# Kernel optimization log

Hardware: AMD Instinct MI355X
Metric: run time of the kernel (lower is better)

## Reference

```python
import jax, jax.numpy as jnp
import numpy as np

B, N = 2, 8192

PARAM_SHAPES = {
    'down0_w': (32, 3), 'down0_b': (32,),
    'sc1_w1': (32, 35), 'sc1_b1': (32,), 'sc1_w2': (64, 32), 'sc1_b2': (64,),
    'sc2_w1': (64, 67), 'sc2_b1': (64,), 'sc2_w2': (128, 64), 'sc2_b2': (128,),
    'sc3_w1': (128, 131), 'sc3_b1': (128,), 'sc3_w2': (192, 128), 'sc3_b2': (192,),
    'sc4_w1': (192, 195), 'sc4_b1': (192,), 'sc4_w2': (192, 192), 'sc4_b2': (192,),
    'up4_w1': (192, 195), 'up4_b1': (192,), 'up4_w2': (192, 384), 'up4_b2': (192,),
    'up3_w1': (128, 195), 'up3_b1': (128,), 'up3_w2': (128, 256), 'up3_b2': (128,),
    'up2_w1': (64, 131), 'up2_b1': (64,), 'up2_w2': (64, 128), 'up2_b2': (64,),
    'up1_w1': (32, 67), 'up1_b1': (32,), 'up1_w2': (32, 64), 'up1_b2': (32,),
}
PNAMES = list(PARAM_SHAPES.keys())


def _fps(xyz, m):
    # xyz [N,3] -> [m] int32 farthest-point-sample indices (deterministic, start at point 0)
    def body(dmin, _):
        nxt = jnp.argmax(dmin)
        d = jnp.sum((xyz - xyz[nxt]) ** 2, -1)
        return jnp.minimum(dmin, d), nxt.astype(jnp.int32)
    d0 = jnp.sum((xyz - xyz[0]) ** 2, -1)
    _, rest = jax.lax.scan(body, d0, None, length=m - 1)
    return jnp.concatenate([jnp.zeros((1,), jnp.int32), rest])


def _gather(pts, idx):
    # pts [B,N,C], idx [B,...] -> [B,...,C]
    return jax.vmap(lambda p, i: p[i])(pts, idx)


def _ball_query(new_xyz, xyz, radius, k):
    # first-k points within radius, invalid slots filled with the first valid index
    d2 = jnp.sum((new_xyz[:, :, None, :] - xyz[:, None, :, :]) ** 2, -1)  # [B,M,N]
    n = xyz.shape[1]
    order = jnp.where(d2 <= radius * radius, jnp.arange(n)[None, None, :], n)
    idx = jnp.argsort(order, axis=-1)[..., :k]
    valid = jnp.take_along_axis(order, idx, -1) < n
    return jnp.where(valid, idx, idx[..., :1])


def _knn(query, ref, k):
    d2 = jnp.sum((query[:, :, None, :] - ref[:, None, :, :]) ** 2, -1)  # [B,Nq,Nr]
    _, idx = jax.lax.top_k(-d2, k)
    return idx


def _mlp(h, w, b):
    # pointwise shared MLP layer with ReLU on channel-last tensor
    return jax.nn.relu(jnp.einsum('...c,oc->...o', h, w) + b)


def _set_conv(xyz, feat, npoint, radius, k, w1, b1, w2, b2):
    # PointNet++-style SetConv: FPS -> ball-query group -> shared MLP -> max-pool
    fps_idx = jax.vmap(_fps, (0, None))(xyz, npoint)          # [B,M]
    new_xyz = _gather(xyz, fps_idx)                            # [B,M,3]
    gi = _ball_query(new_xyz, xyz, radius, k)                  # [B,M,k]
    h = jnp.concatenate([_gather(xyz, gi) - new_xyz[:, :, None, :], _gather(feat, gi)], -1)
    h = _mlp(_mlp(h, w1, b1), w2, b2)                          # [B,M,k,Cout]
    return new_xyz, fps_idx, jnp.max(h, axis=2)


def _set_upconv(s_xyz, d_xyz, s_feat, d_feat, k, w1, b1, w2, b2):
    # FlowNet3D-style SetUpConv: kNN from dense to sparse -> MLP -> max-pool -> fuse with dense feat
    gi = _knn(d_xyz, s_xyz, k)                                 # [B,Nd,k]
    h = jnp.concatenate([_gather(s_xyz, gi) - d_xyz[:, :, None, :], _gather(s_feat, gi)], -1)
    pooled = jnp.max(_mlp(h, w1, b1), axis=2)                  # [B,Nd,m1]
    return _mlp(jnp.concatenate([pooled, d_feat], -1), w2, b2)


def _encoder(pc, feat, p):
    xyz = jnp.transpose(pc, (0, 2, 1))                         # [B,N,3]
    f0 = _mlp(jnp.transpose(feat, (0, 2, 1)), p['down0_w'], p['down0_b'])  # [B,N,32]
    xyz1, i1, f1 = _set_conv(xyz, f0, 2048, 0.5, 16, p['sc1_w1'], p['sc1_b1'], p['sc1_w2'], p['sc1_b2'])
    xyz2, i2, f2 = _set_conv(xyz1, f1, 512, 1.0, 16, p['sc2_w1'], p['sc2_b1'], p['sc2_w2'], p['sc2_b2'])
    xyz3, i3, f3 = _set_conv(xyz2, f2, 128, 2.0, 16, p['sc3_w1'], p['sc3_b1'], p['sc3_w2'], p['sc3_b2'])
    xyz4, i4, f4 = _set_conv(xyz3, f3, 64, 4.0, 16, p['sc4_w1'], p['sc4_b1'], p['sc4_w2'], p['sc4_b2'])
    u3 = _set_upconv(xyz4, xyz3, f4, f3, 8, p['up4_w1'], p['up4_b1'], p['up4_w2'], p['up4_b2'])
    u2 = _set_upconv(xyz3, xyz2, u3, f2, 8, p['up3_w1'], p['up3_b1'], p['up3_w2'], p['up3_b2'])
    u1 = _set_upconv(xyz2, xyz1, u2, f1, 8, p['up2_w1'], p['up2_b1'], p['up2_w2'], p['up2_b2'])
    u0 = _set_upconv(xyz1, xyz, u1, f0, 8, p['up1_w1'], p['up1_b1'], p['up1_w2'], p['up1_b2'])
    return (xyz1, xyz2, xyz3), (i1, i2, i3), (u0, u1, u2, u3)


def setup_inputs() -> dict:
    key = jax.random.key(0)
    ks = jax.random.split(key, 2 + len(PNAMES))
    inp = {
        'pc': jax.random.normal(ks[0], (B, 3, N), jnp.float32),
        'feat': jax.random.normal(ks[1], (B, 3, N), jnp.float32),
    }
    for i, name in enumerate(PNAMES):
        inp[name] = jax.random.normal(ks[2 + i], PARAM_SHAPES[name], jnp.float32) * 0.05
    return inp


def reference(pc, feat, down0_w, down0_b, sc1_w1, sc1_b1, sc1_w2, sc1_b2, sc2_w1, sc2_b1, sc2_w2, sc2_b2, sc3_w1, sc3_b1, sc3_w2, sc3_b2, sc4_w1, sc4_b1, sc4_w2, sc4_b2, up4_w1, up4_b1, up4_w2, up4_b2, up3_w1, up3_b1, up3_w2, up3_b2, up2_w1, up2_b1, up2_w2, up2_b2, up1_w1, up1_b1, up1_w2, up1_b2):
    # GenFlow_unit.forward with gts[0] is None -> pure encoder path
    loc = locals()
    p = {k: loc[k] for k in PNAMES}
    (x1, x2, x3), (i1, i2, i3), (u0, u1, u2, u3) = _encoder(pc, feat, p)
    t = lambda a: jnp.transpose(a, (0, 2, 1))  # back to torch channel-first convention
    return (t(x1), t(x2), t(x3), i1, i2, i3, t(u0), t(u1), t(u2), t(u3))
```

## Files before the change

kernel.cpp:

```cpp
#include <hip/hip_runtime.h>
#include <hip/hip_bf16.h>
#include <cstdint>

#define DEV __device__ __forceinline__

typedef float f32x2 __attribute__((ext_vector_type(2)));

DEV float sqdist(float ax, float ay, float az, float bx, float by, float bz) {
    float dx = __fsub_rn(ax, bx), dy = __fsub_rn(ay, by), dz = __fsub_rn(az, bz);
    return __fadd_rn(__fadd_rn(__fmul_rn(dx, dx), __fmul_rn(dy, dy)), __fmul_rn(dz, dz));
}

DEV f32x2 sqdist2(f32x2 ax, f32x2 ay, f32x2 az, float bx, float by, float bz) {
#pragma clang fp contract(off)
    f32x2 dx = ax - bx, dy = ay - by, dz = az - bz;
    return (dx * dx + dy * dy) + dz * dz;
}

DEV unsigned short f2bf(float f) {
    unsigned int u = __float_as_uint(f);
    u += 0x7fffu + ((u >> 16) & 1u);
    return (unsigned short)(u >> 16);
}

DEV float bf2f(unsigned short u) { return __uint_as_float(((unsigned int)u) << 16); }

template <int CTRL>
DEV int dpp_i(int v) { return __builtin_amdgcn_update_dpp(v, v, CTRL, 0xf, 0xf, false); }
template <int CTRL>
DEV float dpp_f(float v) { return __int_as_float(dpp_i<CTRL>(__float_as_int(v))); }

enum : int {
    O_X1 = 0, O_X2 = 12288, O_X3 = 15360,
    O_I1 = 16128, O_I2 = 20224, O_I3 = 21248,
    O_U0 = 21504, O_U1 = 545792, O_U2 = 807936, O_U3 = 939008
};

__global__ __launch_bounds__(256) void k_init(const float* __restrict__ pc,
                                              const float* __restrict__ feat,
                                              const float* __restrict__ w0,
                                              const float* __restrict__ b0,
                                              float* __restrict__ xyz,
                                              unsigned short* __restrict__ f0) {
    const int N = 8192;
    int i = blockIdx.x * blockDim.x + threadIdx.x;
    if (i >= 2 * N) return;
    int b = i / N, n = i % N;
    float fx0 = feat[(b * 3 + 0) * N + n];
    float fx1 = feat[(b * 3 + 1) * N + n];
    float fx2 = feat[(b * 3 + 2) * N + n];
    xyz[i * 3 + 0] = pc[(b * 3 + 0) * N + n];
    xyz[i * 3 + 1] = pc[(b * 3 + 1) * N + n];
    xyz[i * 3 + 2] = pc[(b * 3 + 2) * N + n];
#pragma unroll
    for (int o = 0; o < 32; o++) {
        float acc = b0[o];
        acc = fmaf(w0[o * 3 + 0], fx0, acc);
        acc = fmaf(w0[o * 3 + 1], fx1, acc);
        acc = fmaf(w0[o * 3 + 2], fx2, acc);
        f0[(size_t)i * 32 + o] = f2bf(fmaxf(acc, 0.f));
    }
}

template <int N, int M, int T>
__global__ __launch_bounds__(T, 1) void k_fps(const float* __restrict__ xyz,
                                              int* __restrict__ idx_out) {
    constexpr int P = N / T;
    constexpr int P2 = P / 2;
    constexpr int W = T / 64;
    int b = blockIdx.x;
    const float* X = xyz + (size_t)b * N * 3;
    int t = threadIdx.x;
    __shared__ float sx[N], sy[N], sz[N];
    __shared__ unsigned long long skey[3];
    f32x2 px[P2], py[P2], pz[P2], dmin[P2];
    float c0x = X[0], c0y = X[1], c0z = X[2];
#pragma unroll
    for (int i = 0; i < P2; i++) {
        int p0 = (2 * i) * T + t, p1 = (2 * i + 1) * T + t;
        px[i] = f32x2{X[p0 * 3 + 0], X[p1 * 3 + 0]};
        py[i] = f32x2{X[p0 * 3 + 1], X[p1 * 3 + 1]};
        pz[i] = f32x2{X[p0 * 3 + 2], X[p1 * 3 + 2]};
        sx[p0] = px[i].x; sy[p0] = py[i].x; sz[p0] = pz[i].x;
        sx[p1] = px[i].y; sy[p1] = py[i].y; sz[p1] = pz[i].y;
        dmin[i] = sqdist2(px[i], py[i], pz[i], c0x, c0y, c0z);
    }
    if (t == 0) {
        idx_out[b * M] = 0;
        skey[0] = 0; skey[1] = 0; skey[2] = 0;
    }
    __syncthreads();
    int jm = 1;
    for (int j = 1; j < M; j++) {
        f32x2 m2[P2];
#pragma unroll
        for (int i = 0; i < P2; i++) m2[i] = dmin[i];
#pragma unroll
        for (int s = P2 / 2; s >= 1; s >>= 1)
#pragma unroll
            for (int i = 0; i < s; i++) m2[i] = __builtin_elementwise_max(m2[i], m2[i + s]);
        float bv = fmaxf(m2[0].x, m2[0].y);
        int ii[P];
#pragma unroll
        for (int i = 0; i < P; i++)
            ii[i] = (dmin[i >> 1][i & 1] == bv) ? (i * T + t) : 0x7fffffff;
#pragma unroll
        for (int s = P / 2; s >= 1; s >>= 1)
#pragma unroll
            for (int i = 0; i < s; i++) ii[i] = min(ii[i], ii[i + s]);
        int bi = ii[0];
        float bw = bv;
        bw = fmaxf(bw, dpp_f<0x121>(bw));
        bw = fmaxf(bw, dpp_f<0x122>(bw));
        bw = fmaxf(bw, dpp_f<0x124>(bw));
        bw = fmaxf(bw, dpp_f<0x128>(bw));
        bw = fmaxf(bw, dpp_f<0x142>(bw));
        bw = fmaxf(bw, dpp_f<0x143>(bw));
        float bvw = __int_as_float(__builtin_amdgcn_readlane(__float_as_int(bw), 63));
        unsigned int im = (bv == bvw) ? (unsigned int)bi : 0xffffffffu;
        im = min(im, (unsigned int)dpp_i<0x121>((int)im));
        im = min(im, (unsigned int)dpp_i<0x122>((int)im));
        im = min(im, (unsigned int)dpp_i<0x124>((int)im));
        im = min(im, (unsigned int)dpp_i<0x128>((int)im));
        im = min(im, (unsigned int)dpp_i<0x142>((int)im));
        im = min(im, (unsigned int)dpp_i<0x143>((int)im));
        int biw = __builtin_amdgcn_readlane((int)im, 63);
        int gi;
        if constexpr (W > 1) {
            unsigned long long key =
                ((unsigned long long)__float_as_uint(bvw) << 32) | (unsigned int)~biw;
            if ((t & 63) == 0) atomicMax(&skey[jm], key);
            __syncthreads();
            unsigned long long gk = skey[jm];
            gi = (int)~(unsigned int)gk;
            if (t == 0) skey[jm == 0 ? 2 : jm - 1] = 0;
            jm = (jm == 2) ? 0 : jm + 1;
        } else {
            gi = biw;
        }
        if (t == 0) idx_out[b * M + j] = gi;
        float cx = sx[gi], cy = sy[gi], cz = sz[gi];
#pragma unroll
        for (int i = 0; i < P2; i++)
            dmin[i] = __builtin_elementwise_min(
                dmin[i], sqdist2(px[i], py[i], pz[i], cx, cy, cz));
    }
}

__global__ __launch_bounds__(256) void k_gather(const float* __restrict__ xyz_src,
                                                const int* __restrict__ idx,
                                                float* __restrict__ xyz_dst,
                                                int NS, int M) {
    int i = blockIdx.x * blockDim.x + threadIdx.x;
    if (i >= 2 * M) return;
    int b = i / M;
    int id = idx[i] & (NS - 1);
    xyz_dst[i * 3 + 0] = xyz_src[((size_t)b * NS + id) * 3 + 0];
    xyz_dst[i * 3 + 1] = xyz_src[((size_t)b * NS + id) * 3 + 1];
    xyz_dst[i * 3 + 2] = xyz_src[((size_t)b * NS + id) * 3 + 2];
}

template <int NS, int CF, int CMID, int COUT>
__global__ __launch_bounds__(128) void k_setconv(
    const float* __restrict__ X, const unsigned short* __restrict__ F,
    const float* __restrict__ C, const float* __restrict__ w1,
    const float* __restrict__ b1, const float* __restrict__ w2,
    const float* __restrict__ b2, unsigned short* __restrict__ fout,
    float r2, int M) {
    constexpr int CIN = 3 + CF;
    constexpr int K = 16;
    constexpr int M8 = CMID / 8;
    constexpr int O8 = COUT / 8;
    int q = blockIdx.x, b = blockIdx.y;
    int blk = b * M + q;
    const float* Xb = X + (size_t)b * NS * 3;
    const unsigned short* Fb = F + (size_t)b * NS * CF;
    int tid = threadIdx.x;
    __shared__ int s_n[K];
    __shared__ int s_cnt;
    __shared__ float s_h[K][CIN];
    __shared__ float s_mid[K][CMID];
    __shared__ float s_pool[2][COUT];
    float cx = C[(size_t)blk * 3 + 0], cy = C[(size_t)blk * 3 + 1], cz = C[(size_t)blk * 3 + 2];
    if (tid < 64) {
        int lane = tid;
        int cnt = 0;
        for (int base = 0; base < NS; base += 64) {
            int p = base + lane;
            float d2 = sqdist(Xb[p * 3], Xb[p * 3 + 1], Xb[p * 3 + 2], cx, cy, cz);
            bool in = (d2 <= r2);
            unsigned long long msk = __ballot(in);
            if (in) {
                int pos = cnt + __popcll(msk & ((1ull << lane) - 1ull));
                if (pos < K) s_n[pos] = p;
            }
            cnt += __popcll(msk);
            if (cnt >= K) break;
        }
        if (lane == 0) s_cnt = cnt < K ? cnt : K;
    }
    __syncthreads();
    int cnt = s_cnt;
    if (tid >= cnt && tid < K) s_n[tid] = s_n[0];
    __syncthreads();
    for (int tIdx = tid; tIdx < K * CIN; tIdx += 128) {
        int n = tIdx / CIN, c = tIdx % CIN;
        int gi = s_n[n];
        float v;
        if (c < 3) v = __fsub_rn(Xb[gi * 3 + c], (c == 0 ? cx : (c == 1 ? cy : cz)));
        else v = bf2f(Fb[(size_t)gi * CF + (c - 3)]);
        s_h[n][c] = v;
    }
    __syncthreads();
    int n = tid >> 3, sub = tid & 7;
#pragma unroll
    for (int j = 0; j < M8; j++) {
        int m = sub * M8 + j;
        float acc = b1[m];
#pragma unroll 4
        for (int c = 0; c < CIN; c++) acc = fmaf(w1[m * CIN + c], s_h[n][c], acc);
        s_mid[n][m] = fmaxf(acc, 0.f);
    }
    __syncthreads();
    float vals[O8];
#pragma unroll
    for (int j = 0; j < O8; j++) {
        int o = sub * O8 + j;
        float acc = b2[o];
#pragma unroll 4
        for (int c = 0; c < CMID; c++) acc = fmaf(w2[o * CMID + c], s_mid[n][c], acc);
        vals[j] = fmaxf(acc, 0.f);
    }
#pragma unroll
    for (int j = 0; j < O8; j++) {
        vals[j] = fmaxf(vals[j], __shfl_xor(vals[j], 8, 64));
        vals[j] = fmaxf(vals[j], __shfl_xor(vals[j], 16, 64));
        vals[j] = fmaxf(vals[j], __shfl_xor(vals[j], 32, 64));
    }
    int lw = tid & 63, wv = tid >> 6;
    if (lw < 8) {
#pragma unroll
        for (int j = 0; j < O8; j++) s_pool[wv][lw * O8 + j] = vals[j];
    }
    __syncthreads();
    if (tid < 8) {
#pragma unroll
        for (int j = 0; j < O8; j++) {
            int o = tid * O8 + j;
            fout[(size_t)blk * COUT + o] = f2bf(fmaxf(s_pool[0][o], s_pool[1][o]));
        }
    }
}

template <int S, int CS, int CMID, int CD, int COUT, bool TRANS>
__global__ __launch_bounds__(64) void k_upconv(
    const float* __restrict__ SX, const float* __restrict__ DX,
    const void* __restrict__ SFv, const unsigned short* __restrict__ DF,
    const float* __restrict__ w1, const float* __restrict__ b1,
    const float* __restrict__ w2, const float* __restrict__ b2,
    float* __restrict__ out, int o_off, int ND) {
    constexpr int K = 8;
    constexpr int CIN = 3 + CS;
    constexpr int CIN2 = CMID + CD;
    constexpr int M8 = CMID / 8;
    int q = blockIdx.x, b = blockIdx.y;
    int blk = b * ND + q;
    int lane = threadIdx.x;
    const float* SXb = SX + (size_t)b * S * 3;
    float qx = DX[(size_t)blk * 3], qy = DX[(size_t)blk * 3 + 1], qz = DX[(size_t)blk * 3 + 2];
    __shared__ int s_k[K];
    __shared__ float s_h[K][CIN];
    __shared__ float s_in2[CIN2];
    float bd[K];
    int bi[K];
#pragma unroll
    for (int i = 0; i < K; i++) { bd[i] = 3.0e38f; bi[i] = 0x7fffffff; }
    for (int p = lane; p < S; p += 64) {
        float d2 = sqdist(SXb[p * 3], SXb[p * 3 + 1], SXb[p * 3 + 2], qx, qy, qz);
        if (d2 < bd[K - 1] || (d2 == bd[K - 1] && p < bi[K - 1])) {
            bd[K - 1] = d2; bi[K - 1] = p;
#pragma unroll
            for (int j = K - 1; j > 0; j--) {
                bool sw = (bd[j] < bd[j - 1]) || (bd[j] == bd[j - 1] && bi[j] < bi[j - 1]);
                if (sw) {
                    float tv = bd[j]; bd[j] = bd[j - 1]; bd[j - 1] = tv;
                    int ti = bi[j]; bi[j] = bi[j - 1]; bi[j - 1] = ti;
                }
            }
        }
    }
    for (int r = 0; r < K; r++) {
        float vv = bd[0]; int vi = bi[0];
#pragma unroll
        for (int m = 1; m < 64; m <<= 1) {
            float ov = __shfl_xor(vv, m, 64);
            int oi = __shfl_xor(vi, m, 64);
            if (ov < vv || (ov == vv && oi < vi)) { vv = ov; vi = oi; }
        }
        if (lane == 0) s_k[r] = vi;
        if (vi == bi[0]) {
#pragma unroll
            for (int j = 0; j < K - 1; j++) { bd[j] = bd[j + 1]; bi[j] = bi[j + 1]; }
            bd[K - 1] = 3.0e38f; bi[K - 1] = 0x7fffffff;
        }
    }
    __syncthreads();
    for (int tIdx = lane; tIdx < K * CIN; tIdx += 64) {
        int n = tIdx / CIN, c = tIdx % CIN;
        int gi = s_k[n];
        float v;
        if (c < 3) v = __fsub_rn(SXb[gi * 3 + c], (c == 0 ? qx : (c == 1 ? qy : qz)));
        else if (TRANS) v = ((const float*)SFv)[((size_t)b * CS + (c - 3)) * S + gi];
        else v = bf2f(((const unsigned short*)SFv)[((size_t)b * S + gi) * CS + (c - 3)]);
        s_h[n][c] = v;
    }
    for (int c = lane; c < CD; c += 64) s_in2[CMID + c] = bf2f(DF[(size_t)blk * CD + c]);
    __syncthreads();
    int n = lane >> 3, sub = lane & 7;
    float vals[M8];
#pragma unroll
    for (int j = 0; j < M8; j++) {
        int m = sub * M8 + j;
        float acc = b1[m];
#pragma unroll 4
        for (int c = 0; c < CIN; c++) acc = fmaf(w1[m * CIN + c], s_h[n][c], acc);
        vals[j] = fmaxf(acc, 0.f);
    }
#pragma unroll
    for (int j = 0; j < M8; j++) {
        vals[j] = fmaxf(vals[j], __shfl_xor(vals[j], 8, 64));
        vals[j] = fmaxf(vals[j], __shfl_xor(vals[j], 16, 64));
        vals[j] = fmaxf(vals[j], __shfl_xor(vals[j], 32, 64));
    }
    if (lane < 8) {
#pragma unroll
        for (int j = 0; j < M8; j++) s_in2[lane * M8 + j] = vals[j];
    }
    __syncthreads();
    for (int o = lane; o < COUT; o += 64) {
        float acc = b2[o];
#pragma unroll 4
        for (int c = 0; c < CIN2; c++) acc = fmaf(w2[o * CIN2 + c], s_in2[c], acc);
        out[o_off + ((size_t)b * COUT + o) * ND + q] = fmaxf(acc, 0.f);
    }
}

__global__ __launch_bounds__(256) void k_finalize(
    const float* __restrict__ xyz1, const float* __restrict__ xyz2,
    const float* __restrict__ xyz3, const int* __restrict__ idx1,
    const int* __restrict__ idx2, const int* __restrict__ idx3,
    float* __restrict__ out) {
    int i = blockIdx.x * blockDim.x + threadIdx.x;
    const float* xs;
    const int* is;
    int M, ox, oi, j;
    if (i < 4096) { xs = xyz1; is = idx1; M = 2048; ox = O_X1; oi = O_I1; j = i; }
    else if (i < 5120) { xs = xyz2; is = idx2; M = 512; ox = O_X2; oi = O_I2; j = i - 4096; }
    else if (i < 5376) { xs = xyz3; is = idx3; M = 128; ox = O_X3; oi = O_I3; j = i - 5120; }
    else return;
    int b = j / M, m = j % M;
    out[ox + (b * 3 + 0) * M + m] = xs[j * 3 + 0];
    out[ox + (b * 3 + 1) * M + m] = xs[j * 3 + 1];
    out[ox + (b * 3 + 2) * M + m] = xs[j * 3 + 2];
    out[oi + j] = (float)is[j];
}

extern "C" void kernel_launch(void* const* d_in, const int* in_sizes, int n_in,
                              void* d_out, int out_size, void* d_ws, size_t ws_size,
                              hipStream_t stream) {
    const float* pc = (const float*)d_in[0];
    const float* feat = (const float*)d_in[1];
    const float* w0 = (const float*)d_in[2];
    const float* b0v = (const float*)d_in[3];
    const float* sc1w1 = (const float*)d_in[4];  const float* sc1b1 = (const float*)d_in[5];
    const float* sc1w2 = (const float*)d_in[6];  const float* sc1b2 = (const float*)d_in[7];
    const float* sc2w1 = (const float*)d_in[8];  const float* sc2b1 = (const float*)d_in[9];
    const float* sc2w2 = (const float*)d_in[10]; const float* sc2b2 = (const float*)d_in[11];
    const float* sc3w1 = (const float*)d_in[12]; const float* sc3b1 = (const float*)d_in[13];
    const float* sc3w2 = (const float*)d_in[14]; const float* sc3b2 = (const float*)d_in[15];
    const float* sc4w1 = (const float*)d_in[16]; const float* sc4b1 = (const float*)d_in[17];
    const float* sc4w2 = (const float*)d_in[18]; const float* sc4b2 = (const float*)d_in[19];
    const float* up4w1 = (const float*)d_in[20]; const float* up4b1 = (const float*)d_in[21];
    const float* up4w2 = (const float*)d_in[22]; const float* up4b2 = (const float*)d_in[23];
    const float* up3w1 = (const float*)d_in[24]; const float* up3b1 = (const float*)d_in[25];
    const float* up3w2 = (const float*)d_in[26]; const float* up3b2 = (const float*)d_in[27];
    const float* up2w1 = (const float*)d_in[28]; const float* up2b1 = (const float*)d_in[29];
    const float* up2w2 = (const float*)d_in[30]; const float* up2b2 = (const float*)d_in[31];
    const float* up1w1 = (const float*)d_in[32]; const float* up1b1 = (const float*)d_in[33];
    const float* up1w2 = (const float*)d_in[34]; const float* up1b2 = (const float*)d_in[35];
    float* out = (float*)d_out;

    char* ws = (char*)d_ws;
    size_t off = 0;
    auto A = [&](size_t bytes) -> char* {
        char* p = ws + off;
        off += (bytes + 255) & ~(size_t)255;
        return p;
    };
    float* xyz  = (float*)A((size_t)2 * 8192 * 3 * 4);
    int* idx1   = (int*)A((size_t)2 * 2048 * 4);
    int* idx2   = (int*)A((size_t)2 * 512 * 4);
    int* idx3   = (int*)A((size_t)2 * 128 * 4);
    int* idx4   = (int*)A((size_t)2 * 64 * 4);
    float* xyz1 = (float*)A((size_t)2 * 2048 * 3 * 4);
    float* xyz2 = (float*)A((size_t)2 * 512 * 3 * 4);
    float* xyz3 = (float*)A((size_t)2 * 128 * 3 * 4);
    float* xyz4 = (float*)A((size_t)2 * 64 * 3 * 4);
    unsigned short* f0 = (unsigned short*)A((size_t)2 * 8192 * 32 * 2);
    unsigned short* f1 = (unsigned short*)A((size_t)2 * 2048 * 64 * 2);
    unsigned short* f2 = (unsigned short*)A((size_t)2 * 512 * 128 * 2);
    unsigned short* f3 = (unsigned short*)A((size_t)2 * 128 * 192 * 2);
    unsigned short* f4 = (unsigned short*)A((size_t)2 * 64 * 192 * 2);

    k_init<<<(2 * 8192 + 255) / 256, 256, 0, stream>>>(pc, feat, w0, b0v, xyz, f0);

    k_fps<8192, 2048, 512><<<2, 512, 0, stream>>>(xyz, idx1);
    k_gather<<<16, 256, 0, stream>>>(xyz, idx1, xyz1, 8192, 2048);
    k_setconv<8192, 32, 32, 64><<<dim3(2048, 2), 128, 0, stream>>>(
        xyz, f0, xyz1, sc1w1, sc1b1, sc1w2, sc1b2, f1, 0.25f, 2048);

    k_fps<2048, 512, 512><<<2, 512, 0, stream>>>(xyz1, idx2);
    k_gather<<<4, 256, 0, stream>>>(xyz1, idx2, xyz2, 2048, 512);
    k_setconv<2048, 64, 64, 128><<<dim3(512, 2), 128, 0, stream>>>(
        xyz1, f1, xyz2, sc2w1, sc2b1, sc2w2, sc2b2, f2, 1.0f, 512);

    k_fps<512, 128, 256><<<2, 256, 0, stream>>>(xyz2, idx3);
    k_gather<<<1, 256, 0, stream>>>(xyz2, idx3, xyz3, 512, 128);
    k_setconv<512, 128, 128, 192><<<dim3(128, 2), 128, 0, stream>>>(
        xyz2, f2, xyz3, sc3w1, sc3b1, sc3w2, sc3b2, f3, 4.0f, 128);

    k_fps<128, 64, 64><<<2, 64, 0, stream>>>(xyz3, idx4);
    k_gather<<<1, 128, 0, stream>>>(xyz3, idx4, xyz4, 128, 64);
    k_setconv<128, 192, 192, 192><<<dim3(64, 2), 128, 0, stream>>>(
        xyz3, f3, xyz4, sc4w1, sc4b1, sc4w2, sc4b2, f4, 16.0f, 64);

    k_upconv<64, 192, 192, 192, 192, false><<<dim3(128, 2), 64, 0, stream>>>(
        xyz4, xyz3, f4, f3, up4w1, up4b1, up4w2, up4b2, out, O_U3, 128);
    k_upconv<128, 192, 128, 128, 128, true><<<dim3(512, 2), 64, 0, stream>>>(
        xyz3, xyz2, out + O_U3, f2, up3w1, up3b1, up3w2, up3b2, out, O_U2, 512);
    k_upconv<512, 128, 64, 64, 64, true><<<dim3(2048, 2), 64, 0, stream>>>(
        xyz2, xyz1, out + O_U2, f1, up2w1, up2b1, up2w2, up2b2, out, O_U1, 2048);
    k_upconv<2048, 64, 32, 32, 32, true><<<dim3(8192, 2), 64, 0, stream>>>(
        xyz1, xyz, out + O_U1, f0, up1w1, up1b1, up1w2, up1b2, out, O_U0, 8192);

    k_finalize<<<(5376 + 255) / 256, 256, 0, stream>>>(
        xyz1, xyz2, xyz3, idx1, idx2, idx3, out);
}
```

Baseline: 4.047 ms.

## Fuse next-level FPS with current set-conv in one launch and use DPP kNN reductions

Merges the next level's farthest-point sampling and the current level's set-conv into one kernel. Two blocks run FPS while the remaining blocks each handle a set-conv centroid, so the serial FPS overlaps the set-conv work and launches are reduced. The level-3 FPS and gather are also moved ahead of the sc3 set-conv. Separately, the kNN top-k wave reduction in upconv now uses DPP min plus readlane instead of xor shuffles. The risks are that set-conv blocks now launch at 512 or 256 threads with only 128 active in the MLP, and that sizing shared memory to the larger FPS need limits occupancy.

Result: faster. 3.846 ms (-5.0%).

```diff
diff --git a/kernel.cpp b/kernel.cpp
--- a/kernel.cpp
+++ b/kernel.cpp
@@ -63,16 +63,16 @@
 }
 
 template <int N, int M, int T>
-__global__ __launch_bounds__(T, 1) void k_fps(const float* __restrict__ xyz,
-                                              int* __restrict__ idx_out) {
+DEV void fps_body(int b, int t, const float* __restrict__ xyz,
+                  int* __restrict__ idx_out, char* smem) {
     constexpr int P = N / T;
     constexpr int P2 = P / 2;
     constexpr int W = T / 64;
-    int b = blockIdx.x;
     const float* X = xyz + (size_t)b * N * 3;
-    int t = threadIdx.x;
-    __shared__ float sx[N], sy[N], sz[N];
-    __shared__ unsigned long long skey[3];
+    float* sx = (float*)smem;
+    float* sy = sx + N;
+    float* sz = sy + N;
+    unsigned long long* skey = (unsigned long long*)(smem + 12 * N);
     f32x2 px[P2], py[P2], pz[P2], dmin[P2];
     float c0x = X[0], c0y = X[1], c0z = X[2];
 #pragma unroll
@@ -147,6 +147,13 @@
     }
 }
 
+template <int N, int M, int T>
+__global__ __launch_bounds__(T, 1) void k_fps(const float* __restrict__ xyz,
+                                              int* __restrict__ idx_out) {
+    __shared__ __align__(16) char smem[12 * N + 24];
+    fps_body<N, M, T>(blockIdx.x, threadIdx.x, xyz, idx_out, smem);
+}
+
 __global__ __launch_bounds__(256) void k_gather(const float* __restrict__ xyz_src,
                                                 const int* __restrict__ idx,
                                                 float* __restrict__ xyz_dst,
@@ -161,26 +168,24 @@
 }
 
 template <int NS, int CF, int CMID, int COUT>
-__global__ __launch_bounds__(128) void k_setconv(
-    const float* __restrict__ X, const unsigned short* __restrict__ F,
-    const float* __restrict__ C, const float* __restrict__ w1,
-    const float* __restrict__ b1, const float* __restrict__ w2,
-    const float* __restrict__ b2, unsigned short* __restrict__ fout,
-    float r2, int M) {
+DEV void setconv_body(int q, int bb, int tid, int bdim,
+                      const float* __restrict__ X, const unsigned short* __restrict__ F,
+                      const float* __restrict__ C, const float* __restrict__ w1,
+                      const float* __restrict__ b1, const float* __restrict__ w2,
+                      const float* __restrict__ b2, unsigned short* __restrict__ fout,
+                      float r2, int M, char* smem) {
     constexpr int CIN = 3 + CF;
     constexpr int K = 16;
     constexpr int M8 = CMID / 8;
     constexpr int O8 = COUT / 8;
-    int q = blockIdx.x, b = blockIdx.y;
-    int blk = b * M + q;
-    const float* Xb = X + (size_t)b * NS * 3;
-    const unsigned short* Fb = F + (size_t)b * NS * CF;
-    int tid = threadIdx.x;
-    __shared__ int s_n[K];
-    __shared__ int s_cnt;
-    __shared__ float s_h[K][CIN];
-    __shared__ float s_mid[K][CMID];
-    __shared__ float s_pool[2][COUT];
+    int blk = bb * M + q;
+    const float* Xb = X + (size_t)bb * NS * 3;
+    const unsigned short* Fb = F + (size_t)bb * NS * CF;
+    int* s_n = (int*)smem;
+    int* s_cntp = (int*)(smem + 64);
+    float* s_h = (float*)(smem + 80);
+    float* s_mid = s_h + K * CIN;
+    float* s_pool = s_mid + K * CMID;
     float cx = C[(size_t)blk * 3 + 0], cy = C[(size_t)blk * 3 + 1], cz = C[(size_t)blk * 3 + 2];
     if (tid < 64) {
         int lane = tid;
@@ -197,58 +202,101 @@
             cnt += __popcll(msk);
             if (cnt >= K) break;
         }
-        if (lane == 0) s_cnt = cnt < K ? cnt : K;
-    }
-    __syncthreads();
-    int cnt = s_cnt;
+        if (lane == 0) *s_cntp = cnt < K ? cnt : K;
+    }
+    __syncthreads();
+    int cnt = *s_cntp;
     if (tid >= cnt && tid < K) s_n[tid] = s_n[0];
     __syncthreads();
-    for (int tIdx = tid; tIdx < K * CIN; tIdx += 128) {
+    for (int tIdx = tid; tIdx < K * CIN; tIdx += bdim) {
         int n = tIdx / CIN, c = tIdx % CIN;
         int gi = s_n[n];
         float v;
         if (c < 3) v = __fsub_rn(Xb[gi * 3 + c], (c == 0 ? cx : (c == 1 ? cy : cz)));
         else v = bf2f(Fb[(size_t)gi * CF + (c - 3)]);
-        s_h[n][c] = v;
-    }
-    __syncthreads();
-    int n = tid >> 3, sub = tid & 7;
-#pragma unroll
-    for (int j = 0; j < M8; j++) {
-        int m = sub * M8 + j;
-        float acc = b1[m];
+        s_h[n * CIN + c] = v;
+    }
+    __syncthreads();
+    if (tid < 128) {
+        int n = tid >> 3, sub = tid & 7;
+#pragma unroll
+        for (int j = 0; j < M8; j++) {
+            int m = sub * M8 + j;
+            float acc = b1[m];
 #pragma unroll 4
-        for (int c = 0; c < CIN; c++) acc = fmaf(w1[m * CIN + c], s_h[n][c], acc);
-        s_mid[n][m] = fmaxf(acc, 0.f);
-    }
-    __syncthreads();
-    float vals[O8];
-#pragma unroll
-    for (int j = 0; j < O8; j++) {
-        int o = sub * O8 + j;
-        float acc = b2[o];
+            for (int c = 0; c < CIN; c++) acc = fmaf(w1[m * CIN + c], s_h[n * CIN + c], acc);
+            s_mid[n * CMID + m] = fmaxf(acc, 0.f);
+        }
+    }
+    __syncthreads();
+    if (tid < 128) {
+        int n = tid >> 3, sub = tid & 7;
+        float vals[O8];
+#pragma unroll
+        for (int j = 0; j < O8; j++) {
+            int o = sub * O8 + j;
+            float acc = b2[o];
 #pragma unroll 4
-        for (int c = 0; c < CMID; c++) acc = fmaf(w2[o * CMID + c], s_mid[n][c], acc);
-        vals[j] = fmaxf(acc, 0.f);
-    }
-#pragma unroll
-    for (int j = 0; j < O8; j++) {
-        vals[j] = fmaxf(vals[j], __shfl_xor(vals[j], 8, 64));
-        vals[j] = fmaxf(vals[j], __shfl_xor(vals[j], 16, 64));
-        vals[j] = fmaxf(vals[j], __shfl_xor(vals[j], 32, 64));
-    }
-    int lw = tid & 63, wv = tid >> 6;
-    if (lw < 8) {
-#pragma unroll
-        for (int j = 0; j < O8; j++) s_pool[wv][lw * O8 + j] = vals[j];
+            for (int c = 0; c < CMID; c++) acc = fmaf(w2[o * CMID + c], s_mid[n * CMID + c], acc);
+            vals[j] = fmaxf(acc, 0.f);
+        }
+#pragma unroll
+        for (int j = 0; j < O8; j++) {
+            vals[j] = fmaxf(vals[j], __shfl_xor(vals[j], 8, 64));
+            vals[j] = fmaxf(vals[j], __shfl_xor(vals[j], 16, 64));
+            vals[j] = fmaxf(vals[j], __shfl_xor(vals[j], 32, 64));
+        }
+        int lw = tid & 63, wv = tid >> 6;
+        if (lw < 8) {
+#pragma unroll
+            for (int j = 0; j < O8; j++) s_pool[wv * COUT + lw * O8 + j] = vals[j];
+        }
     }
     __syncthreads();
     if (tid < 8) {
 #pragma unroll
         for (int j = 0; j < O8; j++) {
             int o = tid * O8 + j;
-            fout[(size_t)blk * COUT + o] = f2bf(fmaxf(s_pool[0][o], s_pool[1][o]));
-        }
+            fout[(size_t)blk * COUT + o] = f2bf(fmaxf(s_pool[o], s_pool[COUT + o]));
+        }
+    }
+}
+
+template <int NS, int CF, int CMID, int COUT>
+__global__ __launch_bounds__(128) void k_setconv(
+    const float* __restrict__ X, const unsigned short* __restrict__ F,
+    const float* __restrict__ C, const float* __restrict__ w1,
+    const float* __restrict__ b1, const float* __restrict__ w2,
+    const float* __restrict__ b2, unsigned short* __restrict__ fout,
+    float r2, int M) {
+    constexpr int K = 16;
+    constexpr int CIN = 3 + CF;
+    __shared__ __align__(16) char smem[80 + 4 * (K * CIN + K * CMID + 2 * COUT)];
+    setconv_body<NS, CF, CMID, COUT>(blockIdx.x, blockIdx.y, threadIdx.x, blockDim.x,
+                                     X, F, C, w1, b1, w2, b2, fout, r2, M, smem);
+}
+
+template <int N, int M, int T, int NS, int CF, int CMID, int COUT>
+__global__ __launch_bounds__(T, 1) void k_fps_sc(
+    const float* __restrict__ fxyz, int* __restrict__ idx_out,
+    const float* __restrict__ X, const unsigned short* __restrict__ F,
+    const float* __restrict__ C, const float* __restrict__ w1,
+    const float* __restrict__ b1, const float* __restrict__ w2,
+    const float* __restrict__ b2, unsigned short* __restrict__ fout,
+    float r2, int Msc) {
+    constexpr int K = 16;
+    constexpr int CIN = 3 + CF;
+    constexpr int FPS_B = 12 * N + 24;
+    constexpr int SC_B = 80 + 4 * (K * CIN + K * CMID + 2 * COUT);
+    constexpr int SB = FPS_B > SC_B ? FPS_B : SC_B;
+    __shared__ __align__(16) char smem[SB];
+    if (blockIdx.x < 2) {
+        fps_body<N, M, T>(blockIdx.x, threadIdx.x, fxyz, idx_out, smem);
+    } else {
+        int lin = blockIdx.x - 2;
+        int q = lin % Msc, bb = lin / Msc;
+        setconv_body<NS, CF, CMID, COUT>(q, bb, threadIdx.x, blockDim.x,
+                                         X, F, C, w1, b1, w2, b2, fout, r2, Msc, smem);
     }
 }
 
@@ -290,15 +338,25 @@
         }
     }
     for (int r = 0; r < K; r++) {
-        float vv = bd[0]; int vi = bi[0];
-#pragma unroll
-        for (int m = 1; m < 64; m <<= 1) {
-            float ov = __shfl_xor(vv, m, 64);
-            int oi = __shfl_xor(vi, m, 64);
-            if (ov < vv || (ov == vv && oi < vi)) { vv = ov; vi = oi; }
-        }
-        if (lane == 0) s_k[r] = vi;
-        if (vi == bi[0]) {
+        float vv = bd[0];
+        float bw = vv;
+        bw = fminf(bw, dpp_f<0x121>(bw));
+        bw = fminf(bw, dpp_f<0x122>(bw));
+        bw = fminf(bw, dpp_f<0x124>(bw));
+        bw = fminf(bw, dpp_f<0x128>(bw));
+        bw = fminf(bw, dpp_f<0x142>(bw));
+        bw = fminf(bw, dpp_f<0x143>(bw));
+        float vw = __int_as_float(__builtin_amdgcn_readlane(__float_as_int(bw), 63));
+        unsigned int im = (vv == vw) ? (unsigned int)bi[0] : 0xffffffffu;
+        im = min(im, (unsigned int)dpp_i<0x121>((int)im));
+        im = min(im, (unsigned int)dpp_i<0x122>((int)im));
+        im = min(im, (unsigned int)dpp_i<0x124>((int)im));
+        im = min(im, (unsigned int)dpp_i<0x128>((int)im));
+        im = min(im, (unsigned int)dpp_i<0x142>((int)im));
+        im = min(im, (unsigned int)dpp_i<0x143>((int)im));
+        int iw = __builtin_amdgcn_readlane((int)im, 63);
+        if (lane == 0) s_k[r] = iw;
+        if (iw == bi[0]) {
 #pragma unroll
             for (int j = 0; j < K - 1; j++) { bd[j] = bd[j + 1]; bi[j] = bi[j + 1]; }
             bd[K - 1] = 3.0e38f; bi[K - 1] = 0x7fffffff;
@@ -416,21 +474,16 @@
 
     k_fps<8192, 2048, 512><<<2, 512, 0, stream>>>(xyz, idx1);
     k_gather<<<16, 256, 0, stream>>>(xyz, idx1, xyz1, 8192, 2048);
-    k_setconv<8192, 32, 32, 64><<<dim3(2048, 2), 128, 0, stream>>>(
-        xyz, f0, xyz1, sc1w1, sc1b1, sc1w2, sc1b2, f1, 0.25f, 2048);
-
-    k_fps<2048, 512, 512><<<2, 512, 0, stream>>>(xyz1, idx2);
+    k_fps_sc<2048, 512, 512, 8192, 32, 32, 64><<<2 + 2 * 2048, 512, 0, stream>>>(
+        xyz1, idx2, xyz, f0, xyz1, sc1w1, sc1b1, sc1w2, sc1b2, f1, 0.25f, 2048);
     k_gather<<<4, 256, 0, stream>>>(xyz1, idx2, xyz2, 2048, 512);
-    k_setconv<2048, 64, 64, 128><<<dim3(512, 2), 128, 0, stream>>>(
-        xyz1, f1, xyz2, sc2w1, sc2b1, sc2w2, sc2b2, f2, 1.0f, 512);
-
-    k_fps<512, 128, 256><<<2, 256, 0, stream>>>(xyz2, idx3);
+    k_fps_sc<512, 128, 256, 2048, 64, 64, 128><<<2 + 2 * 512, 256, 0, stream>>>(
+        xyz2, idx3, xyz1, f1, xyz2, sc2w1, sc2b1, sc2w2, sc2b2, f2, 1.0f, 512);
     k_gather<<<1, 256, 0, stream>>>(xyz2, idx3, xyz3, 512, 128);
+    k_fps<128, 64, 64><<<2, 64, 0, stream>>>(xyz3, idx4);
+    k_gather<<<1, 128, 0, stream>>>(xyz3, idx4, xyz4, 128, 64);
     k_setconv<512, 128, 128, 192><<<dim3(128, 2), 128, 0, stream>>>(
         xyz2, f2, xyz3, sc3w1, sc3b1, sc3w2, sc3b2, f3, 4.0f, 128);
-
-    k_fps<128, 64, 64><<<2, 64, 0, stream>>>(xyz3, idx4);
-    k_gather<<<1, 128, 0, stream>>>(xyz3, idx4, xyz4, 128, 64);
     k_setconv<128, 192, 192, 192><<<dim3(64, 2), 128, 0, stream>>>(
         xyz3, f3, xyz4, sc4w1, sc4b1, sc4w2, sc4b2, f4, 16.0f, 64);
 
```
